# Kernel tuning notes

Hardware: AMD Instinct MI355X
Metric: run time of the kernel (lower is better)

## Reference

```python
import jax, jax.numpy as jnp
import numpy as np

N_FFT = 512
N_STAGES = 4
BASE = N_FFT >> N_STAGES          # base DFT size = 32
SPLIT0 = N_FFT // 2 + 1           # rfft bins = 257
BATCH = 32768


def _mod_seq(order):
    # bit-reversed offset sequence used by get_partial_bit_reversal_matrix
    mset = [0]
    for o in range(order):
        step = 2 ** o
        mset = [v for x in mset for v in (x, x + step)]
    return mset


def _perm_indices():
    # gather indices equivalent to the partial bit-reversal permutation matmul
    base = 2 ** N_STAGES
    n_per = N_FFT // base
    idx = []
    for p in _mod_seq(N_STAGES):
        idx.extend(j * base + p for j in range(n_per))
    return np.asarray(idx, dtype=np.int32)

_PERM_IDX = _perm_indices()
_DFT = np.fft.fft(np.eye(BASE))   # symmetric DFT matrix, M[j,k]=exp(-2pi i jk/BASE)


def setup_inputs() -> dict:
    key = jax.random.key(0)
    x = jax.random.normal(key, (BATCH, N_FFT), dtype=jnp.float32)
    return {"x": x}


def reference(x):
    dt = x.dtype
    dft_r = jnp.asarray(_DFT.real, dtype=dt)
    dft_i = jnp.asarray(_DFT.imag, dtype=dt)

    B = x.shape[0]
    # partial bit-reversal permutation (FFTPermuter) as a gather
    y = x[..., _PERM_IDX].reshape(B, 2 ** N_STAGES, BASE)
    ev = y[:, ::2]   # even-decimated sub-sequences (B, 2^(s-1), BASE)
    od = y[:, 1::2]  # odd-decimated  sub-sequences

    # base-case DFT (DFT module): x @ M with symmetric M
    ev_r = jnp.einsum('bml,lk->bmk', ev, dft_r)
    ev_i = jnp.einsum('bml,lk->bmk', ev, dft_i)
    od_r = jnp.einsum('bml,lk->bmk', od, dft_r)
    od_i = jnp.einsum('bml,lk->bmk', od, dft_i)

    # radix-2 butterfly combine stages (FFTwiddle with SIMPLE ops)
    L = BASE
    for _ in range(N_STAGES):
        w = np.exp(-2j * np.pi * np.arange(L) / (2 * L))
        tw_r = jnp.asarray(w.real, dtype=dt)
        tw_i = jnp.asarray(w.imag, dtype=dt)
        todd_r = tw_r * od_r - tw_i * od_i
        todd_i = tw_r * od_i + tw_i * od_r
        real = jnp.concatenate([ev_r + todd_r, ev_r - todd_r], axis=-1)
        imag = jnp.concatenate([ev_i + todd_i, ev_i - todd_i], axis=-1)
        ev_r, od_r = real[:, ::2], real[:, 1::2]
        ev_i, od_i = imag[:, ::2], imag[:, 1::2]
        L *= 2

    # rfft truncation (torch.split in _RFFTDecompWithGMAC)
    yre = ev_r[:, 0, :SPLIT0]
    yim = ev_i[:, 0, :SPLIT0]
    return (yre, yim)
```

## Files before the change

kernel.cpp:

```cpp
#include <hip/hip_runtime.h>


#define NFFT 512
#define WPB  4

__device__ __forceinline__ int SW(int i) { return i ^ ((i >> 2) & 12); }

__device__ __forceinline__ void waveSyncLds() {
    asm volatile("s_waitcnt lgkmcnt(0)" ::: "memory");
}

__global__ __launch_bounds__(256) void rfft512_kernel(
    const float* __restrict__ x, float* __restrict__ out, int batch)
{
    __shared__ __align__(16) float2 lds[WPB][2][256];
    const int t = threadIdx.x & 63;
    const int w = threadIdx.x >> 6;
    long long b = (long long)blockIdx.x * WPB + w;
    if (b >= batch) b = batch - 1;

    float2* buf0 = lds[w][0];
    float2* buf1 = lds[w][1];

    const float4* xf4 = (const float4*)(x + b * NFFT);
    float4 v0 = xf4[t];
    float4 v1 = xf4[t + 64];
    {
        int p0 = SW(2 * t);
        float4* b4 = (float4*)buf0;
        b4[p0 >> 1]        = v0;
        b4[(p0 >> 1) + 64] = v1;
    }
    waveSyncLds();

    const float NEG2PI = -6.28318530717958647692f;

    {
        int rb = SW(t);
        float2 a = buf0[rb], bb = buf0[rb + 64], c = buf0[rb + 128], d = buf0[rb + 192];
        float apcr = a.x + c.x, apci = a.y + c.y;
        float amcr = a.x - c.x, amci = a.y - c.y;
        float bpdr = bb.x + d.x, bpdi = bb.y + d.y;
        float bmdr = bb.x - d.x, bmdi = bb.y - d.y;
        float y0r = apcr + bpdr, y0i = apci + bpdi;
        float u1r = amcr + bmdi, u1i = amci - bmdr;
        float u2r = apcr - bpdr, u2i = apci - bpdi;
        float u3r = amcr - bmdi, u3i = amci + bmdr;
        float sn, cs;
        __sincosf(NEG2PI * (float)t * (1.0f / 256.0f), &sn, &cs);
        float w1r = cs, w1i = sn;
        float w2r = cs * cs - sn * sn, w2i = 2.0f * cs * sn;
        float w3r = w1r * w2r - w1i * w2i, w3i = w1r * w2i + w1i * w2r;
        int wb = (4 * t) ^ (t & 12);
        float4* d4 = (float4*)buf1;
        d4[wb >> 1]       = make_float4(y0r, y0i,
                                        w1r * u1r - w1i * u1i, w1r * u1i + w1i * u1r);
        d4[(wb >> 1) + 1] = make_float4(w2r * u2r - w2i * u2i, w2r * u2i + w2i * u2r,
                                        w3r * u3r - w3i * u3i, w3r * u3i + w3i * u3r);
    }
    waveSyncLds();

    {
        int rb = SW(t);
        float2 a = buf1[rb], bb = buf1[rb + 64], c = buf1[rb + 128], d = buf1[rb + 192];
        float apcr = a.x + c.x, apci = a.y + c.y;
        float amcr = a.x - c.x, amci = a.y - c.y;
        float bpdr = bb.x + d.x, bpdi = bb.y + d.y;
        float bmdr = bb.x - d.x, bmdi = bb.y - d.y;
        float y0r = apcr + bpdr, y0i = apci + bpdi;
        float u1r = amcr + bmdi, u1i = amci - bmdr;
        float u2r = apcr - bpdr, u2i = apci - bpdi;
        float u3r = amcr - bmdi, u3i = amci + bmdr;
        float sn, cs;
        __sincosf(NEG2PI * (float)(t >> 2) * (1.0f / 64.0f), &sn, &cs);
        float w1r = cs, w1i = sn;
        float w2r = cs * cs - sn * sn, w2i = 2.0f * cs * sn;
        float w3r = w1r * w2r - w1i * w2i, w3i = w1r * w2i + w1i * w2r;
        int wbase = (t & 3) + 16 * (t >> 2);
        buf0[SW(wbase)]      = make_float2(y0r, y0i);
        buf0[SW(wbase + 4)]  = make_float2(w1r * u1r - w1i * u1i, w1r * u1i + w1i * u1r);
        buf0[SW(wbase + 8)]  = make_float2(w2r * u2r - w2i * u2i, w2r * u2i + w2i * u2r);
        buf0[SW(wbase + 12)] = make_float2(w3r * u3r - w3i * u3i, w3r * u3i + w3i * u3r);
    }
    waveSyncLds();

    {
        int rb = SW(t);
        float2 a = buf0[rb], bb = buf0[rb + 64], c = buf0[rb + 128], d = buf0[rb + 192];
        float apcr = a.x + c.x, apci = a.y + c.y;
        float amcr = a.x - c.x, amci = a.y - c.y;
        float bpdr = bb.x + d.x, bpdi = bb.y + d.y;
        float bmdr = bb.x - d.x, bmdi = bb.y - d.y;
        float y0r = apcr + bpdr, y0i = apci + bpdi;
        float u1r = amcr + bmdi, u1i = amci - bmdr;
        float u2r = apcr - bpdr, u2i = apci - bpdi;
        float u3r = amcr - bmdi, u3i = amci + bmdr;
        float sn, cs;
        __sincosf(NEG2PI * (float)(t >> 4) * (1.0f / 16.0f), &sn, &cs);
        float w1r = cs, w1i = sn;
        float w2r = cs * cs - sn * sn, w2i = 2.0f * cs * sn;
        float w3r = w1r * w2r - w1i * w2i, w3i = w1r * w2i + w1i * w2r;
        int wbase = (t & 15) + 64 * (t >> 4);
        buf1[SW(wbase)]      = make_float2(y0r, y0i);
        buf1[SW(wbase + 16)] = make_float2(w1r * u1r - w1i * u1i, w1r * u1i + w1i * u1r);
        buf1[SW(wbase + 32)] = make_float2(w2r * u2r - w2i * u2i, w2r * u2i + w2i * u2r);
        buf1[SW(wbase + 48)] = make_float2(w3r * u3r - w3i * u3i, w3r * u3i + w3i * u3r);
    }
    waveSyncLds();

    float zr[4], zi[4];
    {
        int rb = SW(t);
        float2 a = buf1[rb], bb = buf1[rb + 64], c = buf1[rb + 128], d = buf1[rb + 192];
        float apcr = a.x + c.x, apci = a.y + c.y;
        float amcr = a.x - c.x, amci = a.y - c.y;
        float bpdr = bb.x + d.x, bpdi = bb.y + d.y;
        float bmdr = bb.x - d.x, bmdi = bb.y - d.y;
        zr[0] = apcr + bpdr; zi[0] = apci + bpdi;
        zr[1] = amcr + bmdi; zi[1] = amci - bmdr;
        zr[2] = apcr - bpdr; zi[2] = apci - bpdi;
        zr[3] = amcr - bmdi; zi[3] = amci + bmdr;
        buf0[rb]       = make_float2(zr[0], zi[0]);
        buf0[rb + 64]  = make_float2(zr[1], zi[1]);
        buf0[rb + 128] = make_float2(zr[2], zi[2]);
        buf0[rb + 192] = make_float2(zr[3], zi[3]);
    }
    waveSyncLds();

    float* outRe = out + b * 257;
    float* outIm = out + (long long)batch * 257 + b * 257;
#pragma unroll
    for (int j = 0; j < 4; ++j) {
        int k = t + 64 * j;
        int km = (256 - k) & 255;
        float2 pm = buf0[SW(km)];
        float Ar = 0.5f * (zr[j] + pm.x);
        float Ai = 0.5f * (zi[j] - pm.y);
        float Br = 0.5f * (zi[j] + pm.y);
        float Bi = -0.5f * (zr[j] - pm.x);
        float sn, cs;
        __sincosf(NEG2PI * (float)k * (1.0f / 512.0f), &sn, &cs);
        outRe[k] = Ar + cs * Br - sn * Bi;
        outIm[k] = Ai + cs * Bi + sn * Br;
    }
    if (t == 0) {
        outRe[256] = zr[0] - zi[0];
        outIm[256] = 0.0f;
    }
}

extern "C" void kernel_launch(void* const* d_in, const int* in_sizes, int n_in,
                              void* d_out, int out_size, void* d_ws, size_t ws_size,
                              hipStream_t stream)
{
    const float* x = (const float*)d_in[0];
    float* out = (float*)d_out;
    const int batch = in_sizes[0] / NFFT;
    const int grid = (batch + WPB - 1) / WPB;
    rfft512_kernel<<<grid, 256, 0, stream>>>(x, out, batch);
}
```

Baseline: 116.3 us.

## Load input directly into registers, share twiddles via shuffles, drop final LDS pass

The initial global-to-LDS staging is removed: each thread loads its four radix-4 inputs straight from global memory as float2 and runs the first stage from registers. Twiddles for later stages come from wave shuffles of a single sincos, and the output twiddles are advanced by rotating by -pi/4 per iteration. The final LDS write and read used to fetch mirrored bins is replaced by cross-lane shuffles. This cuts LDS traffic, a wave sync and transcendental calls. In exchange the global loads are narrower float2 accesses instead of float4, and the recurrence-based twiddles may add small rounding error.

```diff
diff --git a/kernel.cpp b/kernel.cpp
--- a/kernel.cpp
+++ b/kernel.cpp
@@ -22,37 +22,31 @@
     float2* buf0 = lds[w][0];
     float2* buf1 = lds[w][1];
 
-    const float4* xf4 = (const float4*)(x + b * NFFT);
-    float4 v0 = xf4[t];
-    float4 v1 = xf4[t + 64];
-    {
-        int p0 = SW(2 * t);
-        float4* b4 = (float4*)buf0;
-        b4[p0 >> 1]        = v0;
-        b4[(p0 >> 1) + 64] = v1;
-    }
-    waveSyncLds();
-
     const float NEG2PI = -6.28318530717958647692f;
 
+    const float2* zin = (const float2*)(x + b * NFFT);
+    float2 a  = zin[t];
+    float2 bb = zin[t + 64];
+    float2 c  = zin[t + 128];
+    float2 d  = zin[t + 192];
+
+    float sA, cA;
+    __sincosf(NEG2PI * (float)t * (1.0f / 256.0f), &sA, &cA);
+
     {
-        int rb = SW(t);
-        float2 a = buf0[rb], bb = buf0[rb + 64], c = buf0[rb + 128], d = buf0[rb + 192];
-        float apcr = a.x + c.x, apci = a.y + c.y;
-        float amcr = a.x - c.x, amci = a.y - c.y;
+        float apcr = a.x + c.x,  apci = a.y + c.y;
+        float amcr = a.x - c.x,  amci = a.y - c.y;
         float bpdr = bb.x + d.x, bpdi = bb.y + d.y;
         float bmdr = bb.x - d.x, bmdi = bb.y - d.y;
         float y0r = apcr + bpdr, y0i = apci + bpdi;
         float u1r = amcr + bmdi, u1i = amci - bmdr;
         float u2r = apcr - bpdr, u2i = apci - bpdi;
         float u3r = amcr - bmdi, u3i = amci + bmdr;
-        float sn, cs;
-        __sincosf(NEG2PI * (float)t * (1.0f / 256.0f), &sn, &cs);
-        float w1r = cs, w1i = sn;
-        float w2r = cs * cs - sn * sn, w2i = 2.0f * cs * sn;
+        float w1r = cA, w1i = sA;
+        float w2r = cA * cA - sA * sA, w2i = 2.0f * cA * sA;
         float w3r = w1r * w2r - w1i * w2i, w3i = w1r * w2i + w1i * w2r;
         int wb = (4 * t) ^ (t & 12);
-        float4* d4 = (float4*)buf1;
+        float4* d4 = (float4*)buf0;
         d4[wb >> 1]       = make_float4(y0r, y0i,
                                         w1r * u1r - w1i * u1i, w1r * u1i + w1i * u1r);
         d4[(wb >> 1) + 1] = make_float4(w2r * u2r - w2i * u2i, w2r * u2i + w2i * u2r,
@@ -62,86 +56,87 @@
 
     {
         int rb = SW(t);
-        float2 a = buf1[rb], bb = buf1[rb + 64], c = buf1[rb + 128], d = buf1[rb + 192];
-        float apcr = a.x + c.x, apci = a.y + c.y;
-        float amcr = a.x - c.x, amci = a.y - c.y;
-        float bpdr = bb.x + d.x, bpdi = bb.y + d.y;
-        float bmdr = bb.x - d.x, bmdi = bb.y - d.y;
+        float2 a2 = buf0[rb], b2 = buf0[rb + 64], c2 = buf0[rb + 128], d2 = buf0[rb + 192];
+        float apcr = a2.x + c2.x, apci = a2.y + c2.y;
+        float amcr = a2.x - c2.x, amci = a2.y - c2.y;
+        float bpdr = b2.x + d2.x, bpdi = b2.y + d2.y;
+        float bmdr = b2.x - d2.x, bmdi = b2.y - d2.y;
         float y0r = apcr + bpdr, y0i = apci + bpdi;
         float u1r = amcr + bmdi, u1i = amci - bmdr;
         float u2r = apcr - bpdr, u2i = apci - bpdi;
         float u3r = amcr - bmdi, u3i = amci + bmdr;
-        float sn, cs;
-        __sincosf(NEG2PI * (float)(t >> 2) * (1.0f / 64.0f), &sn, &cs);
-        float w1r = cs, w1i = sn;
-        float w2r = cs * cs - sn * sn, w2i = 2.0f * cs * sn;
+        float cB = __shfl(cA, t & 60);
+        float sB = __shfl(sA, t & 60);
+        float w1r = cB, w1i = sB;
+        float w2r = cB * cB - sB * sB, w2i = 2.0f * cB * sB;
         float w3r = w1r * w2r - w1i * w2i, w3i = w1r * w2i + w1i * w2r;
         int wbase = (t & 3) + 16 * (t >> 2);
-        buf0[SW(wbase)]      = make_float2(y0r, y0i);
-        buf0[SW(wbase + 4)]  = make_float2(w1r * u1r - w1i * u1i, w1r * u1i + w1i * u1r);
-        buf0[SW(wbase + 8)]  = make_float2(w2r * u2r - w2i * u2i, w2r * u2i + w2i * u2r);
-        buf0[SW(wbase + 12)] = make_float2(w3r * u3r - w3i * u3i, w3r * u3i + w3i * u3r);
+        buf1[SW(wbase)]      = make_float2(y0r, y0i);
+        buf1[SW(wbase + 4)]  = make_float2(w1r * u1r - w1i * u1i, w1r * u1i + w1i * u1r);
+        buf1[SW(wbase + 8)]  = make_float2(w2r * u2r - w2i * u2i, w2r * u2i + w2i * u2r);
+        buf1[SW(wbase + 12)] = make_float2(w3r * u3r - w3i * u3i, w3r * u3i + w3i * u3r);
     }
     waveSyncLds();
 
     {
         int rb = SW(t);
-        float2 a = buf0[rb], bb = buf0[rb + 64], c = buf0[rb + 128], d = buf0[rb + 192];
-        float apcr = a.x + c.x, apci = a.y + c.y;
-        float amcr = a.x - c.x, amci = a.y - c.y;
-        float bpdr = bb.x + d.x, bpdi = bb.y + d.y;
-        float bmdr = bb.x - d.x, bmdi = bb.y - d.y;
+        float2 a2 = buf1[rb], b2 = buf1[rb + 64], c2 = buf1[rb + 128], d2 = buf1[rb + 192];
+        float apcr = a2.x + c2.x, apci = a2.y + c2.y;
+        float amcr = a2.x - c2.x, amci = a2.y - c2.y;
+        float bpdr = b2.x + d2.x, bpdi = b2.y + d2.y;
+        float bmdr = b2.x - d2.x, bmdi = b2.y - d2.y;
         float y0r = apcr + bpdr, y0i = apci + bpdi;
         float u1r = amcr + bmdi, u1i = amci - bmdr;
         float u2r = apcr - bpdr, u2i = apci - bpdi;
         float u3r = amcr - bmdi, u3i = amci + bmdr;
-        float sn, cs;
-        __sincosf(NEG2PI * (float)(t >> 4) * (1.0f / 16.0f), &sn, &cs);
-        float w1r = cs, w1i = sn;
-        float w2r = cs * cs - sn * sn, w2i = 2.0f * cs * sn;
+        float cC = __shfl(cA, t & 48);
+        float sC = __shfl(sA, t & 48);
+        float w1r = cC, w1i = sC;
+        float w2r = cC * cC - sC * sC, w2i = 2.0f * cC * sC;
         float w3r = w1r * w2r - w1i * w2i, w3i = w1r * w2i + w1i * w2r;
         int wbase = (t & 15) + 64 * (t >> 4);
-        buf1[SW(wbase)]      = make_float2(y0r, y0i);
-        buf1[SW(wbase + 16)] = make_float2(w1r * u1r - w1i * u1i, w1r * u1i + w1i * u1r);
-        buf1[SW(wbase + 32)] = make_float2(w2r * u2r - w2i * u2i, w2r * u2i + w2i * u2r);
-        buf1[SW(wbase + 48)] = make_float2(w3r * u3r - w3i * u3i, w3r * u3i + w3i * u3r);
+        buf0[SW(wbase)]      = make_float2(y0r, y0i);
+        buf0[SW(wbase + 16)] = make_float2(w1r * u1r - w1i * u1i, w1r * u1i + w1i * u1r);
+        buf0[SW(wbase + 32)] = make_float2(w2r * u2r - w2i * u2i, w2r * u2i + w2i * u2r);
+        buf0[SW(wbase + 48)] = make_float2(w3r * u3r - w3i * u3i, w3r * u3i + w3i * u3r);
     }
     waveSyncLds();
 
     float zr[4], zi[4];
     {
         int rb = SW(t);
-        float2 a = buf1[rb], bb = buf1[rb + 64], c = buf1[rb + 128], d = buf1[rb + 192];
-        float apcr = a.x + c.x, apci = a.y + c.y;
-        float amcr = a.x - c.x, amci = a.y - c.y;
-        float bpdr = bb.x + d.x, bpdi = bb.y + d.y;
-        float bmdr = bb.x - d.x, bmdi = bb.y - d.y;
+        float2 a2 = buf0[rb], b2 = buf0[rb + 64], c2 = buf0[rb + 128], d2 = buf0[rb + 192];
+        float apcr = a2.x + c2.x, apci = a2.y + c2.y;
+        float amcr = a2.x - c2.x, amci = a2.y - c2.y;
+        float bpdr = b2.x + d2.x, bpdi = b2.y + d2.y;
+        float bmdr = b2.x - d2.x, bmdi = b2.y - d2.y;
         zr[0] = apcr + bpdr; zi[0] = apci + bpdi;
         zr[1] = amcr + bmdi; zi[1] = amci - bmdr;
         zr[2] = apcr - bpdr; zi[2] = apci - bpdi;
         zr[3] = amcr - bmdi; zi[3] = amci + bmdr;
-        buf0[rb]       = make_float2(zr[0], zi[0]);
-        buf0[rb + 64]  = make_float2(zr[1], zi[1]);
-        buf0[rb + 128] = make_float2(zr[2], zi[2]);
-        buf0[rb + 192] = make_float2(zr[3], zi[3]);
     }
-    waveSyncLds();
 
     float* outRe = out + b * 257;
     float* outIm = out + (long long)batch * 257 + b * 257;
+    const int lp = (64 - t) & 63;
+    float sU, cU;
+    __sincosf(NEG2PI * (float)t * (1.0f / 512.0f), &sU, &cU);
+    const float RC = 0.70710678118654752440f;
 #pragma unroll
     for (int j = 0; j < 4; ++j) {
+        float pr = __shfl(zr[3 - j], lp);
+        float pi = __shfl(zi[3 - j], lp);
+        if (t == 0) { pr = zr[(4 - j) & 3]; pi = zi[(4 - j) & 3]; }
         int k = t + 64 * j;
-        int km = (256 - k) & 255;
-        float2 pm = buf0[SW(km)];
-        float Ar = 0.5f * (zr[j] + pm.x);
-        float Ai = 0.5f * (zi[j] - pm.y);
-        float Br = 0.5f * (zi[j] + pm.y);
-        float Bi = -0.5f * (zr[j] - pm.x);
-        float sn, cs;
-        __sincosf(NEG2PI * (float)k * (1.0f / 512.0f), &sn, &cs);
-        outRe[k] = Ar + cs * Br - sn * Bi;
-        outIm[k] = Ai + cs * Bi + sn * Br;
+        float Ar = 0.5f * (zr[j] + pr);
+        float Ai = 0.5f * (zi[j] - pi);
+        float Br = 0.5f * (zi[j] + pi);
+        float Bi = -0.5f * (zr[j] - pr);
+        outRe[k] = Ar + cU * Br - sU * Bi;
+        outIm[k] = Ai + cU * Bi + sU * Br;
+        float nc = RC * (cU + sU);
+        float ns = RC * (sU - cU);
+        cU = nc; sU = ns;
     }
     if (t == 0) {
         outRe[256] = zr[0] - zi[0];
```

New measurement: 111.3 us. 4.2% less time.
